# Kernel tuning notes

Measured on AMD Instinct MI355X. Metric: run time of the kernel, lower is better.

The kernel has to match this reference:

```python
import jax, jax.numpy as jnp
import numpy as np

B, S, H, NH = 1, 2048, 1024, 16
HD = H // NH
LAYER_NUMBER = 1
EPS = 1e-5
NEG_INF = -1e9


def _layernorm(x, g, b):
    mu = jnp.mean(x, axis=-1, keepdims=True)
    var = jnp.mean((x - mu) ** 2, axis=-1, keepdims=True)
    return (x - mu) * jax.lax.rsqrt(var + EPS) * g + b


def _bloom_gelu(x):
    # tanh approximation used by Megatron/Bloom
    return x * 0.5 * (1.0 + jnp.tanh(0.79788456 * x * (1.0 + 0.044715 * x * x)))


def setup_inputs() -> dict:
    key = jax.random.key(0)
    ks = jax.random.split(key, 8)

    def w(k, shape, scale=0.02):
        return jax.random.normal(k, shape, jnp.float32) * scale

    # additive causal mask: 0 where attended, -1e9 where masked
    causal = jnp.where(jnp.tril(jnp.ones((S, S), bool)), 0.0, NEG_INF).astype(jnp.float32)
    attention_mask = causal[None, None]  # [1,1,S,S]

    return {
        "hidden_states": jax.random.normal(ks[0], (B, S, H), jnp.float32),
        "attention_mask": attention_mask,
        "alibi": w(ks[1], (B * NH, 1, S), 1.0),
        "ln1_g": jnp.ones((H,), jnp.float32),
        "ln1_b": jnp.zeros((H,), jnp.float32),
        "qkv_w": w(ks[2], (3 * H, H)),
        "qkv_b": jnp.zeros((3 * H,), jnp.float32),
        "dense_w": w(ks[3], (H, H)),
        "dense_b": jnp.zeros((H,), jnp.float32),
        "ln2_g": jnp.ones((H,), jnp.float32),
        "ln2_b": jnp.zeros((H,), jnp.float32),
        "fc1_w": w(ks[4], (4 * H, H)),
        "fc1_b": jnp.zeros((4 * H,), jnp.float32),
        "fc2_w": w(ks[5], (H, 4 * H)),
        "fc2_b": jnp.zeros((H,), jnp.float32),
    }


def reference(hidden_states, attention_mask, alibi,
              ln1_g, ln1_b, qkv_w, qkv_b, dense_w, dense_b,
              ln2_g, ln2_b, fc1_w, fc1_b, fc2_w, fc2_b):
    dtype = hidden_states.dtype
    norm_factor = np.sqrt(HD).astype(np.float32) * LAYER_NUMBER
    beta = 1.0 / LAYER_NUMBER

    # --- input layernorm (residual = pre-LN hidden states) ---
    ln_out = _layernorm(hidden_states, ln1_g, ln1_b)
    residual = hidden_states

    # --- attention ---
    fused = ln_out @ qkv_w.T + qkv_b                      # [B,S,3H]
    fused = fused.reshape(B, S, NH, 3 * HD)
    q, k, v = fused[..., :HD], fused[..., HD:2 * HD], fused[..., 2 * HD:]

    scores = jnp.einsum('bqhd,bkhd->bhqk', q, k) / norm_factor \
             + beta * alibi.reshape(B, NH, 1, S)          # [B,NH,S,S]
    attn = scores * LAYER_NUMBER + attention_mask
    attn = jnp.maximum(attn, jnp.finfo(attn.dtype).min)
    probs = jax.nn.softmax(attn.astype(jnp.float32), axis=-1).astype(dtype)
    probs = probs * (attention_mask == 0.0)               # zero out masked positions

    ctx = jnp.einsum('bhqk,bkhd->bqhd', probs, v).reshape(B, S, H)
    attn_out = ctx @ dense_w.T + dense_b + residual       # dropout_add, p=0

    # --- post-attention layernorm + MLP ---
    ln2_out = _layernorm(attn_out, ln2_g, ln2_b)
    residual2 = attn_out
    h = _bloom_gelu(ln2_out @ fc1_w.T + fc1_b)            # [B,S,4H]
    out = h @ fc2_w.T + fc2_b + residual2                 # dropout_add, p=0
    return out
```

## Files before the change

### kernel.cpp

```cpp
#include <hip/hip_runtime.h>
#include <hip/hip_bf16.h>

typedef unsigned short u16;
typedef __attribute__((ext_vector_type(8))) short bf16x8;
typedef __attribute__((ext_vector_type(4))) float f32x4;

typedef __attribute__((address_space(1))) const void cgvoid;
typedef __attribute__((address_space(3))) void lvoid;

static __device__ __forceinline__ u16 f2bf(float x) {
    __hip_bfloat16 h = __float2bfloat16(x);
    return __builtin_bit_cast(u16, h);
}
static __device__ __forceinline__ float bf2f(u16 x) {
    return __builtin_bit_cast(float, ((unsigned)x) << 16);
}

static __device__ __forceinline__ void gload_lds16(const u16* g, u16* l) {
    __builtin_amdgcn_global_load_lds((cgvoid*)g, (lvoid*)l, 16, 0, 0);
}

__global__ __launch_bounds__(256) void prep(
    const float* __restrict__ hidden, const float* __restrict__ g1,
    const float* __restrict__ b1, u16* __restrict__ ln_out,
    const float* __restrict__ qkv_w, const float* __restrict__ dense_w,
    const float* __restrict__ fc1_w, const float* __restrict__ fc2_w,
    u16* __restrict__ qkv_wb, u16* __restrict__ dense_wb,
    u16* __restrict__ fc1_wb, u16* __restrict__ fc2_wb)
{
    const int t = threadIdx.x;
    if (blockIdx.x < 2048) {
        const int row = blockIdx.x;
        const float4 v = ((const float4*)(hidden + (size_t)row * 1024))[t];
        float s  = v.x + v.y + v.z + v.w;
        float sq = v.x*v.x + v.y*v.y + v.z*v.z + v.w*v.w;
#pragma unroll
        for (int d = 1; d < 64; d <<= 1) {
            s  += __shfl_xor(s, d, 64);
            sq += __shfl_xor(sq, d, 64);
        }
        __shared__ float ss[4], ssq[4];
        const int wave = t >> 6, lane = t & 63;
        if (lane == 0) { ss[wave] = s; ssq[wave] = sq; }
        __syncthreads();
        s  = ss[0] + ss[1] + ss[2] + ss[3];
        sq = ssq[0] + ssq[1] + ssq[2] + ssq[3];
        const float mu = s * (1.f / 1024.f);
        const float rinv = rsqrtf(sq * (1.f / 1024.f) - mu * mu + 1e-5f);
        const float4 gv = ((const float4*)g1)[t];
        const float4 bv = ((const float4*)b1)[t];
        ushort4 pk;
        pk.x = f2bf((v.x - mu) * rinv * gv.x + bv.x);
        pk.y = f2bf((v.y - mu) * rinv * gv.y + bv.y);
        pk.z = f2bf((v.z - mu) * rinv * gv.z + bv.z);
        pk.w = f2bf((v.w - mu) * rinv * gv.w + bv.w);
        ((ushort4*)(ln_out + (size_t)row * 1024))[t] = pk;
        return;
    }
    constexpr int C0 = 786432;
    constexpr int C1 = C0 + 262144;
    constexpr int C2 = C1 + 1048576;
    constexpr int C3 = C2 + 1048576;
    int i = (blockIdx.x - 2048) * 256 + t;
    const int stride = (gridDim.x - 2048) * 256;
    for (; i < C3; i += stride) {
        const float* src; u16* dst; int j;
        if (i < C0)      { src = qkv_w;   dst = qkv_wb;   j = i; }
        else if (i < C1) { src = dense_w; dst = dense_wb; j = i - C0; }
        else if (i < C2) { src = fc1_w;   dst = fc1_wb;   j = i - C1; }
        else             { src = fc2_w;   dst = fc2_wb;   j = i - C2; }
        const float4 v = ((const float4*)src)[j];
        ushort4 pk;
        pk.x = f2bf(v.x); pk.y = f2bf(v.y); pk.z = f2bf(v.z); pk.w = f2bf(v.w);
        ((ushort4*)dst)[j] = pk;
    }
}

template<int EPI, int BM, int BN>
__global__ __launch_bounds__(256, (BN == 128) ? 3 : 4) void gemm_bt(
    const u16* __restrict__ A, const u16* __restrict__ Bw,
    const float* __restrict__ bias, void* __restrict__ Cout,
    u16* __restrict__ p0, u16* __restrict__ pext,
    u16* __restrict__ qPo, u16* __restrict__ kPo, u16* __restrict__ vPo,
    int M, int N, int K, int Kspan)
{
    constexpr int WC = BN / 64;
    constexpr int WR = 4 / WC;
    constexpr int MI = BM / (WR * 16);
    constexpr int NI = 4;
    __shared__ __align__(16) u16 As[BM * 64];
    __shared__ __align__(16) u16 Bs[BN * 64];
    const int t = threadIdx.x;
    const int lane = t & 63;
    const int wave = t >> 6;
    const int wr = wave / WC, wc = wave % WC;
    const int g = lane >> 4, r16 = lane & 15;

    const int nxy = gridDim.x * gridDim.y;
    const int bid0 = blockIdx.x + gridDim.x * blockIdx.y;
    const int v = (bid0 & 7) * (nxy >> 3) + (bid0 >> 3);
    const int tile_m = (v / gridDim.y) * BM;
    const int tile_n = (v % gridDim.y) * BN;
    const int kb = blockIdx.z * Kspan;

    f32x4 acc[MI][NI] = {};

    for (int k0 = kb; k0 < kb + Kspan; k0 += 64) {
        __syncthreads();
#pragma unroll
        for (int i = 0; i < BM / 32; ++i) {
            const int off = (t + i * 256) * 8;
            gload_lds16(A + (size_t)(tile_m + (off >> 6)) * K + k0 + (off & 63), As + off);
        }
#pragma unroll
        for (int i = 0; i < BN / 32; ++i) {
            const int off = (t + i * 256) * 8;
            gload_lds16(Bw + (size_t)(tile_n + (off >> 6)) * K + k0 + (off & 63), Bs + off);
        }
        __syncthreads();

        bf16x8 af[MI][2], bfr[NI][2];
#pragma unroll
        for (int mi = 0; mi < MI; ++mi)
#pragma unroll
            for (int ks = 0; ks < 2; ++ks)
                af[mi][ks] = *(const bf16x8*)(As + (wr*(MI*16) + mi*16 + r16)*64 + ks*32 + g*8);
#pragma unroll
        for (int ni = 0; ni < NI; ++ni)
#pragma unroll
            for (int ks = 0; ks < 2; ++ks)
                bfr[ni][ks] = *(const bf16x8*)(Bs + (wc*64 + ni*16 + r16)*64 + ks*32 + g*8);
#pragma unroll
        for (int mi = 0; mi < MI; ++mi)
#pragma unroll
            for (int ni = 0; ni < NI; ++ni) {
                acc[mi][ni] = __builtin_amdgcn_mfma_f32_16x16x32_bf16(af[mi][0], bfr[ni][0], acc[mi][ni], 0, 0, 0);
                acc[mi][ni] = __builtin_amdgcn_mfma_f32_16x16x32_bf16(af[mi][1], bfr[ni][1], acc[mi][ni], 0, 0, 0);
            }
    }

    u16* dst = nullptr;
    if constexpr (EPI == 4)
        dst = (blockIdx.z == 0) ? p0 : pext + (size_t)(blockIdx.z - 1) * ((size_t)M * N);

#pragma unroll
    for (int mi = 0; mi < MI; ++mi) {
#pragma unroll
        for (int ni = 0; ni < NI; ++ni) {
            const int col = tile_n + wc*64 + ni*16 + r16;
            const int row0 = tile_m + wr*(MI*16) + mi*16 + g*4;
            float vv[4];
#pragma unroll
            for (int r = 0; r < 4; ++r) {
                if constexpr (EPI == 4) vv[r] = acc[mi][ni][r];
                else                    vv[r] = acc[mi][ni][r] + bias[col];
            }
            if constexpr (EPI != 3) {
#pragma unroll
                for (int r = 0; r < 4; ++r) {
                    const int row = row0 + r;
                    if constexpr (EPI == 4) {
                        dst[(size_t)row * N + col] = f2bf(vv[r]);
                    } else if constexpr (EPI == 0) {
                        ((u16*)Cout)[(size_t)row * N + col] = f2bf(vv[r]);
                    } else {
                        const float c = 0.79788456f * vv[r] * (1.0f + 0.044715f * vv[r] * vv[r]);
                        ((u16*)Cout)[(size_t)row * N + col] = f2bf(vv[r] / (1.0f + __expf(-2.0f * c)));
                    }
                }
            } else {
                const int h = col / 192;
                const int fm = col % 192;
                if ((fm >> 6) == 0) {
                    const int f = fm;
                    const int ks = f >> 5, gg = (f >> 3) & 3, e = f & 7;
#pragma unroll
                    for (int r = 0; r < 4; ++r) {
                        const int tkn = row0 + r;
                        const int qt = tkn >> 4, rr = tkn & 15;
                        qPo[((size_t)(h*128 + qt)*2 + ks)*512 + (gg*16 + rr)*8 + e] = f2bf(vv[r]);
                    }
                } else if ((fm >> 6) == 1) {
                    const int f = fm - 64;
                    const int ks = f >> 5, gg = (f >> 3) & 3, e = f & 7;
#pragma unroll
                    for (int r = 0; r < 4; ++r) {
                        const int tkn = row0 + r;
                        const int kt = tkn >> 6, w = tkn & 63;
                        const int kn = ((w >> 5) << 1) | ((w >> 2) & 1);
                        const int rp = ((w >> 3) & 3) * 4 + (w & 3);
                        kPo[((size_t)(h*32 + kt))*4096 + (kn*2 + ks)*512 + (gg*16 + rp)*8 + e] = f2bf(vv[r]);
                    }
                } else {
                    const int f = fm - 128;
                    const int nd = f >> 4, rv = f & 15;
                    const int kt = row0 >> 6, w = row0 & 63;
                    const int ks = w >> 5, gg = (w >> 3) & 3, e0 = w & 7;
                    ushort4 pk4;
                    pk4.x = f2bf(vv[0]); pk4.y = f2bf(vv[1]);
                    pk4.z = f2bf(vv[2]); pk4.w = f2bf(vv[3]);
                    *(ushort4*)(vPo + ((size_t)(h*32 + kt))*4096 + (nd*2 + ks)*512 + (gg*16 + rv)*8 + e0) = pk4;
                }
            }
        }
    }
}

__global__ __launch_bounds__(256) void reduce2_ln(
    const u16* __restrict__ p0, const u16* __restrict__ p1,
    const float* __restrict__ bias, const float* __restrict__ res,
    float* __restrict__ attn_o, const float* __restrict__ g2,
    const float* __restrict__ b2, u16* __restrict__ ln_out)
{
    const int row = blockIdx.x;
    const int t = threadIdx.x;
    const size_t i = (size_t)row * 256 + t;
    const ushort4 a0 = ((const ushort4*)p0)[i];
    const ushort4 a1 = ((const ushort4*)p1)[i];
    const float4 bv = ((const float4*)bias)[t];
    const float4 rv = ((const float4*)res)[i];
    float4 v;
    v.x = bf2f(a0.x) + bf2f(a1.x) + bv.x + rv.x;
    v.y = bf2f(a0.y) + bf2f(a1.y) + bv.y + rv.y;
    v.z = bf2f(a0.z) + bf2f(a1.z) + bv.z + rv.z;
    v.w = bf2f(a0.w) + bf2f(a1.w) + bv.w + rv.w;
    ((float4*)attn_o)[i] = v;

    float s  = v.x + v.y + v.z + v.w;
    float sq = v.x*v.x + v.y*v.y + v.z*v.z + v.w*v.w;
#pragma unroll
    for (int d = 1; d < 64; d <<= 1) {
        s  += __shfl_xor(s, d, 64);
        sq += __shfl_xor(sq, d, 64);
    }
    __shared__ float ss[4], ssq[4];
    const int wave = t >> 6, lane = t & 63;
    if (lane == 0) { ss[wave] = s; ssq[wave] = sq; }
    __syncthreads();
    s  = ss[0] + ss[1] + ss[2] + ss[3];
    sq = ssq[0] + ssq[1] + ssq[2] + ssq[3];
    const float mu = s * (1.f / 1024.f);
    const float rinv = rsqrtf(sq * (1.f / 1024.f) - mu * mu + 1e-5f);
    const float4 gv = ((const float4*)g2)[t];
    const float4 b2v = ((const float4*)b2)[t];
    ushort4 pk;
    pk.x = f2bf((v.x - mu) * rinv * gv.x + b2v.x);
    pk.y = f2bf((v.y - mu) * rinv * gv.y + b2v.y);
    pk.z = f2bf((v.z - mu) * rinv * gv.z + b2v.z);
    pk.w = f2bf((v.w - mu) * rinv * gv.w + b2v.w);
    ((ushort4*)(ln_out + (size_t)row * 1024))[t] = pk;
}

template<int NP>
__global__ __launch_bounds__(256) void reduce_bias_res(
    const u16* __restrict__ p0, const u16* __restrict__ pext,
    const float* __restrict__ bias, const float* __restrict__ res,
    float* __restrict__ out, int n4, int n4row)
{
    int i = blockIdx.x * blockDim.x + threadIdx.x;
    const int stride = gridDim.x * blockDim.x;
    for (; i < n4; i += stride) {
        const ushort4 a0 = ((const ushort4*)p0)[i];
        float ax = bf2f(a0.x), ay = bf2f(a0.y), az = bf2f(a0.z), aw = bf2f(a0.w);
#pragma unroll
        for (int j = 0; j < NP - 1; ++j) {
            const ushort4 b = ((const ushort4*)pext)[(size_t)j * n4 + i];
            ax += bf2f(b.x); ay += bf2f(b.y); az += bf2f(b.z); aw += bf2f(b.w);
        }
        const float4 bv = ((const float4*)bias)[i & (n4row - 1)];
        const float4 rv = ((const float4*)res)[i];
        float4 o;
        o.x = ax + bv.x + rv.x;
        o.y = ay + bv.y + rv.y;
        o.z = az + bv.z + rv.z;
        o.w = aw + bv.w + rv.w;
        ((float4*)out)[i] = o;
    }
}

__global__ __launch_bounds__(256, 4) void attn_swapped(
    const u16* __restrict__ qP, const u16* __restrict__ kP,
    const u16* __restrict__ vP, const float* __restrict__ alibi,
    u16* __restrict__ ctx)
{
    const int bid = blockIdx.x;
    const int h = bid & 15;
    const int qt = 127 - (bid >> 4);
    const int qw0 = qt * 16;
    const int t = threadIdx.x;
    const int lane = t & 63, wave = t >> 6;
    const int g = lane >> 4, r16 = lane & 15;
    const int qrow = qw0 + r16;

    __shared__ float Ms[4][16], Ls[4][16];
    __shared__ float Os[4][4][16][17];

    bf16x8 qf[2];
    qf[0] = *(const bf16x8*)(qP + ((size_t)(h*128 + qt)*2 + 0)*512 + lane*8);
    qf[1] = *(const bf16x8*)(qP + ((size_t)(h*128 + qt)*2 + 1)*512 + lane*8);

    f32x4 o_acc[4] = {};
    float m_r = -3.0e38f, l_r = 0.f;

    const u16* kPh = kP + (size_t)h * 32 * 4096;
    const u16* vPh = vP + (size_t)h * 32 * 4096;
    const float* abase = alibi + (size_t)h * 2048;

    const int nkt = (qw0 >> 6) + 1;
    for (int kt = wave; kt < nkt; kt += 4) {
        const int kt0 = kt * 64;
        const u16* kT = kPh + (size_t)kt * 4096;
        const u16* vT = vPh + (size_t)kt * 4096;

        bf16x8 kf[4][2], vf[4][2];
#pragma unroll
        for (int kn = 0; kn < 4; ++kn) {
            kf[kn][0] = *(const bf16x8*)(kT + (kn*2 + 0)*512 + lane*8);
            kf[kn][1] = *(const bf16x8*)(kT + (kn*2 + 1)*512 + lane*8);
        }
        float4 al[4];
#pragma unroll
        for (int kn = 0; kn < 4; ++kn)
            al[kn] = *(const float4*)(abase + kt0 + 32*(kn>>1) + 8*g + 4*(kn&1));
#pragma unroll
        for (int nd = 0; nd < 4; ++nd) {
            vf[nd][0] = *(const bf16x8*)(vT + (nd*2 + 0)*512 + lane*8);
            vf[nd][1] = *(const bf16x8*)(vT + (nd*2 + 1)*512 + lane*8);
        }

        f32x4 sc[4] = {};
#pragma unroll
        for (int kn = 0; kn < 4; ++kn) {
            sc[kn] = __builtin_amdgcn_mfma_f32_16x16x32_bf16(kf[kn][0], qf[0], sc[kn], 0, 0, 0);
            sc[kn] = __builtin_amdgcn_mfma_f32_16x16x32_bf16(kf[kn][1], qf[1], sc[kn], 0, 0, 0);
        }

        float s[4][4];
        float rmax = -3.0e38f;
#pragma unroll
        for (int kn = 0; kn < 4; ++kn) {
            const int kb = kt0 + 32*(kn>>1) + 8*g + 4*(kn&1);
            const float alv[4] = {al[kn].x, al[kn].y, al[kn].z, al[kn].w};
#pragma unroll
            for (int r = 0; r < 4; ++r) {
                float v = sc[kn][r] * 0.125f + alv[r];
                v = (kb + r <= qrow) ? v : -1.0e30f;
                s[kn][r] = v;
                rmax = fmaxf(rmax, v);
            }
        }
        rmax = fmaxf(rmax, __shfl_xor(rmax, 16, 64));
        rmax = fmaxf(rmax, __shfl_xor(rmax, 32, 64));

        const float mnew = fmaxf(m_r, rmax);
        const float scale = __expf(m_r - mnew);
        m_r = mnew;

        float psum = 0.f;
        u16 ph[4][4];
#pragma unroll
        for (int kn = 0; kn < 4; ++kn)
#pragma unroll
            for (int r = 0; r < 4; ++r) {
                const float p = __expf(s[kn][r] - mnew);
                psum += p;
                ph[kn][r] = f2bf(p);
            }
        psum += __shfl_xor(psum, 16, 64);
        psum += __shfl_xor(psum, 32, 64);
        l_r = l_r * scale + psum;

#pragma unroll
        for (int nd = 0; nd < 4; ++nd)
#pragma unroll
            for (int r = 0; r < 4; ++r)
                o_acc[nd][r] *= scale;

        bf16x8 pf[2];
#pragma unroll
        for (int ks = 0; ks < 2; ++ks) {
            union { bf16x8 v; u16 e[8]; } u;
#pragma unroll
            for (int r = 0; r < 4; ++r) { u.e[r] = ph[2*ks][r]; u.e[4+r] = ph[2*ks+1][r]; }
            pf[ks] = u.v;
        }
#pragma unroll
        for (int nd = 0; nd < 4; ++nd) {
            o_acc[nd] = __builtin_amdgcn_mfma_f32_16x16x32_bf16(vf[nd][0], pf[0], o_acc[nd], 0, 0, 0);
            o_acc[nd] = __builtin_amdgcn_mfma_f32_16x16x32_bf16(vf[nd][1], pf[1], o_acc[nd], 0, 0, 0);
        }
    }

#pragma unroll
    for (int nd = 0; nd < 4; ++nd)
#pragma unroll
        for (int r = 0; r < 4; ++r)
            Os[wave][nd][g*4 + r][r16] = o_acc[nd][r];
    if (g == 0) { Ms[wave][r16] = m_r; Ls[wave][r16] = l_r; }
    __syncthreads();

    if (wave == 0) {
        const float m0 = Ms[0][r16], m1 = Ms[1][r16], m2 = Ms[2][r16], m3 = Ms[3][r16];
        const float ms = fmaxf(fmaxf(m0, m1), fmaxf(m2, m3));
        const float f0 = __expf(m0 - ms), f1 = __expf(m1 - ms);
        const float f2 = __expf(m2 - ms), f3 = __expf(m3 - ms);
        const float l = f0*Ls[0][r16] + f1*Ls[1][r16] + f2*Ls[2][r16] + f3*Ls[3][r16];
        const float inv = 1.0f / l;
#pragma unroll
        for (int nd = 0; nd < 4; ++nd) {
            float v[4];
#pragma unroll
            for (int r = 0; r < 4; ++r) {
                const int d = g*4 + r;
                v[r] = (f0*Os[0][nd][d][r16] + f1*Os[1][nd][d][r16] +
                        f2*Os[2][nd][d][r16] + f3*Os[3][nd][d][r16]) * inv;
            }
            ushort4 pk;
            pk.x = f2bf(v[0]); pk.y = f2bf(v[1]); pk.z = f2bf(v[2]); pk.w = f2bf(v[3]);
            *(ushort4*)(ctx + (size_t)qrow * 1024 + h*64 + nd*16 + g*4) = pk;
        }
    }
}

extern "C" void kernel_launch(void* const* d_in, const int* in_sizes, int n_in,
                              void* d_out, int out_size, void* d_ws, size_t ws_size,
                              hipStream_t stream)
{
    (void)in_sizes; (void)n_in; (void)out_size; (void)ws_size;
    const float* hidden  = (const float*)d_in[0];
    const float* alibi   = (const float*)d_in[2];
    const float* ln1_g   = (const float*)d_in[3];
    const float* ln1_b   = (const float*)d_in[4];
    const float* qkv_w   = (const float*)d_in[5];
    const float* qkv_b   = (const float*)d_in[6];
    const float* dense_w = (const float*)d_in[7];
    const float* dense_b = (const float*)d_in[8];
    const float* ln2_g   = (const float*)d_in[9];
    const float* ln2_b   = (const float*)d_in[10];
    const float* fc1_w   = (const float*)d_in[11];
    const float* fc1_b   = (const float*)d_in[12];
    const float* fc2_w   = (const float*)d_in[13];
    const float* fc2_b   = (const float*)d_in[14];
    float* out = (float*)d_out;

    char* p = (char*)d_ws;
    u16* ln_buf   = (u16*)p;  p += (size_t)2048 * 1024 * 2;
    u16* qkv_wb   = (u16*)p;  p += (size_t)3072 * 1024 * 2;
    u16* qP       = (u16*)p;  p += (size_t)2048 * 3072 * 2;
    u16* ctx      = (u16*)p;  p += (size_t)2048 * 1024 * 2;
    u16* dense_wb = (u16*)p;  p += (size_t)1024 * 1024 * 2;
    float* attn_o = (float*)p; p += (size_t)2048 * 1024 * 4;
    u16* fc1_wb   = (u16*)p;  p += (size_t)4096 * 1024 * 2;
    u16* fc2_wb   = (u16*)p;  p += (size_t)1024 * 4096 * 2;
    u16* pext     = (u16*)p;  p += (size_t)3 * 2048 * 1024 * 2;
    u16* part0    = (u16*)p;  p += (size_t)2048 * 1024 * 2;
    u16* hbuf = qP;
    u16* kP = (u16*)attn_o;
    u16* vP = kP + (size_t)16 * 32 * 4096;

    prep<<<6144, 256, 0, stream>>>(hidden, ln1_g, ln1_b, ln_buf,
                                   qkv_w, dense_w, fc1_w, fc2_w,
                                   qkv_wb, dense_wb, fc1_wb, fc2_wb);
    gemm_bt<3,128,64><<<dim3(16, 48), 256, 0, stream>>>(ln_buf, qkv_wb, qkv_b, nullptr,
                                                        nullptr, nullptr, qP, kP, vP,
                                                        2048, 3072, 1024, 1024);
    attn_swapped<<<2048, 256, 0, stream>>>(qP, kP, vP, alibi, ctx);
    gemm_bt<4,128,64><<<dim3(16, 16, 2), 256, 0, stream>>>(ctx, dense_wb, nullptr, nullptr,
                                                           part0, pext, nullptr, nullptr, nullptr,
                                                           2048, 1024, 1024, 512);
    reduce2_ln<<<2048, 256, 0, stream>>>(part0, pext, dense_b, hidden, attn_o,
                                         ln2_g, ln2_b, ln_buf);
    gemm_bt<2,128,128><<<dim3(16, 32), 256, 0, stream>>>(ln_buf, fc1_wb, fc1_b, hbuf,
                                                         nullptr, nullptr, nullptr, nullptr, nullptr,
                                                         2048, 4096, 1024, 1024);
    gemm_bt<4,128,128><<<dim3(16, 8, 4), 256, 0, stream>>>(hbuf, fc2_wb, nullptr, nullptr,
                                                           part0, pext, nullptr, nullptr, nullptr,
                                                           2048, 1024, 4096, 1024);
    reduce_bias_res<4><<<2048, 256, 0, stream>>>(part0, pext, fc2_b, attn_o, out,
                                                 2048*1024/4, 256);
}
```

Before: 156.1 us.

## Fuse dense bias+residual into GEMM epilogue, store attn_out bf16, prioritize MFMA waves

```diff
diff --git a/kernel.cpp b/kernel.cpp
--- a/kernel.cpp
+++ b/kernel.cpp
@@ -79,7 +79,8 @@
 template<int EPI, int BM, int BN>
 __global__ __launch_bounds__(256, (BN == 128) ? 3 : 4) void gemm_bt(
     const u16* __restrict__ A, const u16* __restrict__ Bw,
-    const float* __restrict__ bias, void* __restrict__ Cout,
+    const float* __restrict__ bias, const float* __restrict__ resi,
+    void* __restrict__ Cout,
     u16* __restrict__ p0, u16* __restrict__ pext,
     u16* __restrict__ qPo, u16* __restrict__ kPo, u16* __restrict__ vPo,
     int M, int N, int K, int Kspan)
@@ -163,6 +164,9 @@
                         dst[(size_t)row * N + col] = f2bf(vv[r]);
                     } else if constexpr (EPI == 0) {
                         ((u16*)Cout)[(size_t)row * N + col] = f2bf(vv[r]);
+                    } else if constexpr (EPI == 5) {
+                        ((u16*)Cout)[(size_t)row * N + col] =
+                            f2bf(vv[r] + resi[(size_t)row * N + col]);
                     } else {
                         const float c = 0.79788456f * vv[r] * (1.0f + 0.044715f * vv[r] * vv[r]);
                         ((u16*)Cout)[(size_t)row * N + col] = f2bf(vv[r] / (1.0f + __expf(-2.0f * c)));
@@ -206,25 +210,15 @@
     }
 }
 
-__global__ __launch_bounds__(256) void reduce2_ln(
-    const u16* __restrict__ p0, const u16* __restrict__ p1,
-    const float* __restrict__ bias, const float* __restrict__ res,
-    float* __restrict__ attn_o, const float* __restrict__ g2,
+__global__ __launch_bounds__(256) void ln2_bf16(
+    const u16* __restrict__ x, const float* __restrict__ g2,
     const float* __restrict__ b2, u16* __restrict__ ln_out)
 {
     const int row = blockIdx.x;
     const int t = threadIdx.x;
-    const size_t i = (size_t)row * 256 + t;
-    const ushort4 a0 = ((const ushort4*)p0)[i];
-    const ushort4 a1 = ((const ushort4*)p1)[i];
-    const float4 bv = ((const float4*)bias)[t];
-    const float4 rv = ((const float4*)res)[i];
+    const ushort4 xa = ((const ushort4*)(x + (size_t)row * 1024))[t];
     float4 v;
-    v.x = bf2f(a0.x) + bf2f(a1.x) + bv.x + rv.x;
-    v.y = bf2f(a0.y) + bf2f(a1.y) + bv.y + rv.y;
-    v.z = bf2f(a0.z) + bf2f(a1.z) + bv.z + rv.z;
-    v.w = bf2f(a0.w) + bf2f(a1.w) + bv.w + rv.w;
-    ((float4*)attn_o)[i] = v;
+    v.x = bf2f(xa.x); v.y = bf2f(xa.y); v.z = bf2f(xa.z); v.w = bf2f(xa.w);
 
     float s  = v.x + v.y + v.z + v.w;
     float sq = v.x*v.x + v.y*v.y + v.z*v.z + v.w*v.w;
@@ -254,7 +248,7 @@
 template<int NP>
 __global__ __launch_bounds__(256) void reduce_bias_res(
     const u16* __restrict__ p0, const u16* __restrict__ pext,
-    const float* __restrict__ bias, const float* __restrict__ res,
+    const float* __restrict__ bias, const u16* __restrict__ res,
     float* __restrict__ out, int n4, int n4row)
 {
     int i = blockIdx.x * blockDim.x + threadIdx.x;
@@ -268,12 +262,12 @@
             ax += bf2f(b.x); ay += bf2f(b.y); az += bf2f(b.z); aw += bf2f(b.w);
         }
         const float4 bv = ((const float4*)bias)[i & (n4row - 1)];
-        const float4 rv = ((const float4*)res)[i];
+        const ushort4 rv = ((const ushort4*)res)[i];
         float4 o;
-        o.x = ax + bv.x + rv.x;
-        o.y = ay + bv.y + rv.y;
-        o.z = az + bv.z + rv.z;
-        o.w = aw + bv.w + rv.w;
+        o.x = ax + bv.x + bf2f(rv.x);
+        o.y = ay + bv.y + bf2f(rv.y);
+        o.z = az + bv.z + bf2f(rv.z);
+        o.w = aw + bv.w + bf2f(rv.w);
         ((float4*)out)[i] = o;
     }
 }
@@ -329,11 +323,13 @@
         }
 
         f32x4 sc[4] = {};
+        __builtin_amdgcn_s_setprio(1);
 #pragma unroll
         for (int kn = 0; kn < 4; ++kn) {
             sc[kn] = __builtin_amdgcn_mfma_f32_16x16x32_bf16(kf[kn][0], qf[0], sc[kn], 0, 0, 0);
             sc[kn] = __builtin_amdgcn_mfma_f32_16x16x32_bf16(kf[kn][1], qf[1], sc[kn], 0, 0, 0);
         }
+        __builtin_amdgcn_s_setprio(0);
 
         float s[4][4];
         float rmax = -3.0e38f;
@@ -384,11 +380,13 @@
             for (int r = 0; r < 4; ++r) { u.e[r] = ph[2*ks][r]; u.e[4+r] = ph[2*ks+1][r]; }
             pf[ks] = u.v;
         }
+        __builtin_amdgcn_s_setprio(1);
 #pragma unroll
         for (int nd = 0; nd < 4; ++nd) {
             o_acc[nd] = __builtin_amdgcn_mfma_f32_16x16x32_bf16(vf[nd][0], pf[0], o_acc[nd], 0, 0, 0);
             o_acc[nd] = __builtin_amdgcn_mfma_f32_16x16x32_bf16(vf[nd][1], pf[1], o_acc[nd], 0, 0, 0);
         }
+        __builtin_amdgcn_s_setprio(0);
     }
 
 #pragma unroll
@@ -449,31 +447,31 @@
     u16* qP       = (u16*)p;  p += (size_t)2048 * 3072 * 2;
     u16* ctx      = (u16*)p;  p += (size_t)2048 * 1024 * 2;
     u16* dense_wb = (u16*)p;  p += (size_t)1024 * 1024 * 2;
-    float* attn_o = (float*)p; p += (size_t)2048 * 1024 * 4;
+    u16* kvbuf    = (u16*)p;  p += (size_t)2048 * 1024 * 4;
     u16* fc1_wb   = (u16*)p;  p += (size_t)4096 * 1024 * 2;
     u16* fc2_wb   = (u16*)p;  p += (size_t)1024 * 4096 * 2;
     u16* pext     = (u16*)p;  p += (size_t)3 * 2048 * 1024 * 2;
     u16* part0    = (u16*)p;  p += (size_t)2048 * 1024 * 2;
     u16* hbuf = qP;
-    u16* kP = (u16*)attn_o;
+    u16* kP = kvbuf;
     u16* vP = kP + (size_t)16 * 32 * 4096;
+    u16* attn_o = kvbuf;
 
     prep<<<6144, 256, 0, stream>>>(hidden, ln1_g, ln1_b, ln_buf,
                                    qkv_w, dense_w, fc1_w, fc2_w,
                                    qkv_wb, dense_wb, fc1_wb, fc2_wb);
-    gemm_bt<3,128,64><<<dim3(16, 48), 256, 0, stream>>>(ln_buf, qkv_wb, qkv_b, nullptr,
+    gemm_bt<3,128,64><<<dim3(16, 48), 256, 0, stream>>>(ln_buf, qkv_wb, qkv_b, nullptr, nullptr,
                                                         nullptr, nullptr, qP, kP, vP,
                                                         2048, 3072, 1024, 1024);
     attn_swapped<<<2048, 256, 0, stream>>>(qP, kP, vP, alibi, ctx);
-    gemm_bt<4,128,64><<<dim3(16, 16, 2), 256, 0, stream>>>(ctx, dense_wb, nullptr, nullptr,
-                                                           part0, pext, nullptr, nullptr, nullptr,
-                                                           2048, 1024, 1024, 512);
-    reduce2_ln<<<2048, 256, 0, stream>>>(part0, pext, dense_b, hidden, attn_o,
-                                         ln2_g, ln2_b, ln_buf);
-    gemm_bt<2,128,128><<<dim3(16, 32), 256, 0, stream>>>(ln_buf, fc1_wb, fc1_b, hbuf,
+    gemm_bt<5,64,64><<<dim3(32, 16), 256, 0, stream>>>(ctx, dense_wb, dense_b, hidden, attn_o,
+                                                       nullptr, nullptr, nullptr, nullptr, nullptr,
+                                                       2048, 1024, 1024, 1024);
+    ln2_bf16<<<2048, 256, 0, stream>>>(attn_o, ln2_g, ln2_b, ln_buf);
+    gemm_bt<2,128,128><<<dim3(16, 32), 256, 0, stream>>>(ln_buf, fc1_wb, fc1_b, nullptr, hbuf,
                                                          nullptr, nullptr, nullptr, nullptr, nullptr,
                                                          2048, 4096, 1024, 1024);
-    gemm_bt<4,128,128><<<dim3(16, 8, 4), 256, 0, stream>>>(hbuf, fc2_wb, nullptr, nullptr,
+    gemm_bt<4,128,128><<<dim3(16, 8, 4), 256, 0, stream>>>(hbuf, fc2_wb, nullptr, nullptr, nullptr,
                                                            part0, pext, nullptr, nullptr, nullptr,
                                                            2048, 1024, 4096, 1024);
     reduce_bias_res<4><<<2048, 256, 0, stream>>>(part0, pext, fc2_b, attn_o, out,
```

After: 157.9 us. Within noise of the previous version (+1.2%).
